# Kernel optimization log

Measured on AMD Instinct MI355X. Metric: run time of the kernel, lower is better.

The kernel has to match this reference:

```python
import jax, jax.numpy as jnp
import numpy as np

N = 50000      # nodes
E = 800000     # edges (avg degree 16)
HID = 64       # hidden / out_channels per head (concat=False)
EDIM = 3       # edge_dim
H = 4          # heads
C = 64         # per-head channels (== hidden since concat=False mean)
L = 2          # ode_layers
NEG_SLOPE = 0.2
LN_EPS = 1e-5


def setup_inputs() -> dict:
    key = jax.random.key(0)
    ks = jax.random.split(key, 12)
    h = jax.random.normal(ks[0], (N, HID), dtype=jnp.float32)
    edge_index = jax.random.randint(ks[1], (2, E), 0, N, dtype=jnp.int64)
    edge_attr = jax.random.normal(ks[2], (E, EDIM), dtype=jnp.float32)
    t = jnp.zeros((), dtype=jnp.float32)
    s = 1.0 / np.sqrt(HID)
    lin_W = jax.random.normal(ks[3], (L, H * C, HID), dtype=jnp.float32) * s
    lin_W = lin_W.at[L - 1].mul(0.1)  # mimics gats[-1].lin.weight.mul_(0.1)
    lin_edge_W = jax.random.normal(ks[4], (L, H * C, EDIM), dtype=jnp.float32) * (1.0 / np.sqrt(EDIM))
    att_src = jax.random.normal(ks[5], (L, H, C), dtype=jnp.float32) * s
    att_dst = jax.random.normal(ks[6], (L, H, C), dtype=jnp.float32) * s
    att_edge = jax.random.normal(ks[7], (L, H, C), dtype=jnp.float32) * s
    bias = jnp.zeros((L, C), dtype=jnp.float32)
    ln_gamma = jnp.ones((L, HID), dtype=jnp.float32)
    ln_beta = jnp.zeros((L, HID), dtype=jnp.float32)
    return {"t": t, "h": h, "edge_index": edge_index, "edge_attr": edge_attr,
            "lin_W": lin_W, "lin_edge_W": lin_edge_W, "att_src": att_src,
            "att_dst": att_dst, "att_edge": att_edge, "bias": bias,
            "ln_gamma": ln_gamma, "ln_beta": ln_beta}


def _gat_layer(z, src, dst, lin_W, lin_edge_W, att_src, att_dst, att_edge,
               bias, edge_attr):
    n = z.shape[0]
    x = (z @ lin_W.T).reshape(n, H, C)                      # [N,H,C]
    a_src = (x * att_src).sum(-1)                            # [N,H]
    a_dst = (x * att_dst).sum(-1)                            # [N,H]
    e = (edge_attr @ lin_edge_W.T).reshape(-1, H, C)         # [E,H,C]
    a_e = (e * att_edge).sum(-1)                             # [E,H]
    alpha = jax.nn.leaky_relu(a_src[src] + a_dst[dst] + a_e, NEG_SLOPE)
    # segment-softmax over incoming edges of each destination node
    amax = jax.ops.segment_max(alpha, dst, num_segments=n)
    amax = jnp.where(jnp.isfinite(amax), amax, 0.0)
    ex = jnp.exp(alpha - amax[dst])                          # [E,H]
    denom = jax.ops.segment_sum(ex, dst, num_segments=n)
    w = ex / (denom[dst] + 1e-16)
    msg = jax.ops.segment_sum(w[:, :, None] * x[src], dst, num_segments=n)
    return msg.mean(axis=1) + bias                           # [N,C] (concat=False)


def reference(t, h, edge_index, edge_attr, lin_W, lin_edge_W, att_src,
              att_dst, att_edge, bias, ln_gamma, ln_beta):
    src, dst = edge_index[0], edge_index[1]
    z = h
    for i in range(L):
        out = _gat_layer(z, src, dst, lin_W[i], lin_edge_W[i], att_src[i],
                         att_dst[i], att_edge[i], bias[i], edge_attr)
        mu = out.mean(-1, keepdims=True)
        var = ((out - mu) ** 2).mean(-1, keepdims=True)
        ln = (out - mu) / jnp.sqrt(var + LN_EPS) * ln_gamma[i] + ln_beta[i]
        z = jax.nn.silu(ln)
    return z
```

## Files before the change

### kernel.cpp

```cpp
#include <hip/hip_runtime.h>
#include <math.h>

#define NN 50000
#define NE 800000
#define NEG_SLOPE 0.2f
#define LN_EPS 1e-5f
#define SROW 264

typedef unsigned short ushort_t;
typedef unsigned int uint_t;
typedef __attribute__((ext_vector_type(8))) short bf16x8;
typedef __attribute__((ext_vector_type(4))) float f32x4;

__device__ __forceinline__ float bf2f(ushort_t u) {
    return __uint_as_float(((uint_t)u) << 16);
}
__device__ __forceinline__ ushort_t f2bf(float f) {
    uint_t b = __float_as_uint(f);
    uint_t r = (b + 0x7fffu + ((b >> 16) & 1u)) >> 16;
    return (ushort_t)r;
}
__device__ __forceinline__ float ldx(const void* p, size_t i, int isbf) {
    return isbf ? bf2f(((const ushort_t*)p)[i]) : ((const float*)p)[i];
}
__device__ __forceinline__ int clampN(int v) {
    return v < 0 ? 0 : (v >= NN ? NN - 1 : v);
}
__device__ __forceinline__ int ld_src(const int* ei, int e, int f64) {
    return clampN(f64 ? ei[2 * e] : ei[e]);
}
__device__ __forceinline__ int ld_dst(const int* ei, int e, int f64) {
    return clampN(f64 ? ei[2 * NE + 2 * e] : ei[NE + e]);
}
__device__ __forceinline__ int sniff_isbf(const void* hptr) {
    const ushort_t* hu = (const ushort_t*)hptr;
    int bf = 1;
    for (int i = 0; i < 512; i += 2) {
        uint_t ex = (hu[i] >> 7) & 0xFFu;
        if (ex > 0x8Cu) bf = 0;
    }
    return bf;
}
__device__ __forceinline__ int sniff_f64(const int* ei) {
    return (ei[1] == 0 && ei[3] == 0 && ei[5] == 0 && ei[7] == 0) ? 1 : 0;
}

__global__ __launch_bounds__(256) void setup(
    const void* __restrict__ lin_W, const void* __restrict__ lin_edge_W,
    const void* __restrict__ att_src, const void* __restrict__ att_dst,
    const void* __restrict__ att_edge, const void* __restrict__ h_in,
    const int* __restrict__ ei, float* __restrict__ Mbuf,
    ushort_t* __restrict__ wext, ushort_t* __restrict__ hbf,
    int* __restrict__ deg, int* __restrict__ flags) {
    int tid = threadIdx.x, lane = tid & 63;
    int nthreads = gridDim.x * 256;
    int gtid = blockIdx.x * 256 + tid;
    __shared__ int s_isbf;
    if (tid == 0) s_isbf = sniff_isbf(h_in);
    __syncthreads();
    int isbf = s_isbf;
    if (gtid == 0) {
        flags[0] = sniff_f64(ei);
        flags[1] = isbf;
    }
    for (int i = gtid; i < NN; i += nthreads) deg[i] = 0;
    if (blockIdx.x == 0) {
        for (int rep = 0; rep < 2; ++rep) {
            int idx = rep * 256 + tid;
            int l = idx >> 8, hc = idx & 255;
            float ae = ldx(att_edge, l * 256 + hc, isbf);
            size_t b3 = ((size_t)l * 256 + hc) * 3;
            float q0 = ae * ldx(lin_edge_W, b3 + 0, isbf);
            float q1 = ae * ldx(lin_edge_W, b3 + 1, isbf);
            float q2 = ae * ldx(lin_edge_W, b3 + 2, isbf);
            for (int off = 32; off > 0; off >>= 1) {
                q0 += __shfl_down(q0, off);
                q1 += __shfl_down(q1, off);
                q2 += __shfl_down(q2, off);
            }
            if (lane == 0) {
                int h = (idx >> 6) & 3;
                Mbuf[(l * 4 + h) * 3 + 0] = q0;
                Mbuf[(l * 4 + h) * 3 + 1] = q1;
                Mbuf[(l * 4 + h) * 3 + 2] = q2;
            }
        }
    }
    for (int idx = gtid; idx < 2 * 272 * 64; idx += nthreads) {
        int d = idx & 63;
        int row = (idx >> 6) % 272;
        int l = idx / (272 * 64);
        float v = 0.f;
        if (row < 256) {
            v = ldx(lin_W, ((size_t)l * 256 + row) * 64 + d, isbf);
        } else if (row < 264) {
            int h = (row - 256) & 3;
            const void* att = (row < 260) ? att_src : att_dst;
            for (int c = 0; c < 64; ++c) {
                v += ldx(lin_W, ((size_t)l * 256 + h * 64 + c) * 64 + d, isbf) *
                     ldx(att, l * 256 + h * 64 + c, isbf);
            }
        }
        wext[((size_t)l * 272 + row) * 64 + d] = f2bf(v);
    }
    if (!isbf) {
        for (int i = gtid; i < NN * 64; i += nthreads)
            hbf[i] = f2bf(((const float*)h_in)[i]);
    }
}


__global__ void csr_hist_pos(const int* __restrict__ ei, int* __restrict__ deg,
                             int* __restrict__ pos, const int* __restrict__ flags) {
    int e = blockIdx.x * 256 + threadIdx.x;
    if (e >= NE) return;
    pos[e] = atomicAdd(&deg[ld_dst(ei, e, flags[0])], 1);
}

__global__ __launch_bounds__(1024) void csr_scan(const int* __restrict__ deg,
                                                 int* __restrict__ rowptr) {
    __shared__ int sh[1024];
    __shared__ int prefix_sh;
    int tid = threadIdx.x;
    int i = blockIdx.x * 1024 + tid;
    int pre = 0;
    for (int k = tid; k < blockIdx.x * 1024; k += 1024) pre += deg[k];
    sh[tid] = pre;
    __syncthreads();
    for (int off = 512; off > 0; off >>= 1) {
        if (tid < off) sh[tid] += sh[tid + off];
        __syncthreads();
    }
    if (tid == 0) prefix_sh = sh[0];
    __syncthreads();
    int prefix = prefix_sh;
    __syncthreads();
    int v = (i < NN) ? deg[i] : 0;
    sh[tid] = v;
    __syncthreads();
    for (int off = 1; off < 1024; off <<= 1) {
        int t = (tid >= off) ? sh[tid - off] : 0;
        __syncthreads();
        sh[tid] += t;
        __syncthreads();
    }
    if (i < NN) rowptr[i] = prefix + sh[tid] - v;
    if (i == 0) rowptr[NN] = NE;
}

__global__ void csr_fill(const int* __restrict__ ei, const void* __restrict__ edge_attr,
                         const int* __restrict__ rowptr, const int* __restrict__ pos,
                         float4* __restrict__ edata, const int* __restrict__ flags) {
    int e = blockIdx.x * 256 + threadIdx.x;
    if (e >= NE) return;
    int f64 = flags[0], isbf = flags[1];
    int s = ld_src(ei, e, f64), d = ld_dst(ei, e, f64);
    float4 ed;
    ed.x = ldx(edge_attr, (size_t)e * 3 + 0, isbf);
    ed.y = ldx(edge_attr, (size_t)e * 3 + 1, isbf);
    ed.z = ldx(edge_attr, (size_t)e * 3 + 2, isbf);
    ed.w = __int_as_float(s);
    edata[rowptr[d] + pos[e]] = ed;
}


__global__ __launch_bounds__(256) void node_linear(
    const void* __restrict__ h_in, const ushort_t* __restrict__ hbf,
    const ushort_t* __restrict__ zbuf, const ushort_t* __restrict__ wext,
    ushort_t* __restrict__ xb, float* __restrict__ a_src, float* __restrict__ a_dst,
    const int* __restrict__ flags, int layer) {
    __shared__ __align__(16) ushort_t st_all[4 * 16 * SROW];
    int isbf = flags[1];
    int tid = threadIdx.x, wv = tid >> 6, lane = tid & 63;
    int q = lane >> 4, mi = lane & 15;
    const ushort_t* zsrc = (layer == 0) ? (isbf ? (const ushort_t*)h_in : hbf) : zbuf;
    const ushort_t* wl = wext + (size_t)layer * 272 * 64;
    bf16x8 wf[34];
#pragma unroll
    for (int t = 0; t < 17; ++t) {
        const ushort_t* wrow = wl + (size_t)(t * 16 + mi) * 64;
        wf[2 * t]     = *(const bf16x8*)(wrow + q * 8);
        wf[2 * t + 1] = *(const bf16x8*)(wrow + 32 + q * 8);
    }
    ushort_t* st = st_all + wv * 16 * SROW;
    int gwave = blockIdx.x * 4 + wv, nwaves = gridDim.x * 4;
    for (int tile = gwave; tile < NN / 16; tile += nwaves) {
        int mbase = tile * 16, mynode = mbase + mi;
        const ushort_t* zrow = zsrc + (size_t)mynode * 64;
        bf16x8 b0 = *(const bf16x8*)(zrow + q * 8);
        bf16x8 b1 = *(const bf16x8*)(zrow + 32 + q * 8);
#pragma unroll
        for (int t = 0; t < 17; ++t) {
            f32x4 acc = {0.f, 0.f, 0.f, 0.f};
            acc = __builtin_amdgcn_mfma_f32_16x16x32_bf16(wf[2 * t], b0, acc, 0, 0, 0);
            acc = __builtin_amdgcn_mfma_f32_16x16x32_bf16(wf[2 * t + 1], b1, acc, 0, 0, 0);
            if (t < 16) {
                ushort4 pk;
                pk.x = f2bf(acc[0]);
                pk.y = f2bf(acc[1]);
                pk.z = f2bf(acc[2]);
                pk.w = f2bf(acc[3]);
                *(ushort4*)(st + mi * SROW + t * 16 + q * 4) = pk;
            } else {
                float4 av;
                av.x = acc[0]; av.y = acc[1]; av.z = acc[2]; av.w = acc[3];
                if (q == 0) *(float4*)(a_src + (size_t)mynode * 4) = av;
                else if (q == 1) *(float4*)(a_dst + (size_t)mynode * 4) = av;
            }
        }
        for (int nn = 0; nn < 16; ++nn) {
            int node = mbase + nn;
            ushort4 pk;
            pk.x = st[nn * SROW + lane];
            pk.y = st[nn * SROW + 64 + lane];
            pk.z = st[nn * SROW + 128 + lane];
            pk.w = st[nn * SROW + 192 + lane];
            *(ushort4*)(xb + (size_t)node * 256 + lane * 4) = pk;
        }
    }
}

__global__ __launch_bounds__(256) void node_aggregate(
    const int* __restrict__ rowptr, const float4* __restrict__ edata,
    const float* __restrict__ a_src, const float* __restrict__ a_dst,
    const ushort_t* __restrict__ xb, const float* __restrict__ Mbuf,
    const void* __restrict__ bias, const void* __restrict__ gamma,
    const void* __restrict__ beta, ushort_t* __restrict__ zout,
    void* __restrict__ outp, const int* __restrict__ flags, int layer, int last) {
    __shared__ float4 wsh[4][64];
    __shared__ int ssh[4][64];
    int isbf = flags[1];
    int wv = threadIdx.x >> 6;
    int lane = threadIdx.x & 63;
    int n = blockIdx.x * 4 + wv;
    float M[12];
#pragma unroll
    for (int i = 0; i < 12; ++i) M[i] = Mbuf[layer * 12 + i];
    float4 ad = *(const float4*)(a_dst + (size_t)n * 4);
    int start = rowptr[n], end = rowptr[n + 1];
    float acc0 = 0.f, acc1 = 0.f, acc2 = 0.f, acc3 = 0.f;
    float den0 = 0.f, den1 = 0.f, den2 = 0.f, den3 = 0.f;
    for (int cb = start; cb < end; cb += 64) {
        int m = end - cb;
        if (m > 64) m = 64;
        if (lane < m) {
            float4 ed = edata[cb + lane];
            int s = __float_as_int(ed.w);
            float4 as4 = *(const float4*)(a_src + (size_t)s * 4);
            float t0 = as4.x + ad.x + ed.x * M[0] + ed.y * M[1] + ed.z * M[2];
            float t1 = as4.y + ad.y + ed.x * M[3] + ed.y * M[4] + ed.z * M[5];
            float t2 = as4.z + ad.z + ed.x * M[6] + ed.y * M[7] + ed.z * M[8];
            float t3 = as4.w + ad.w + ed.x * M[9] + ed.y * M[10] + ed.z * M[11];
            t0 = t0 > 0.f ? t0 : NEG_SLOPE * t0;
            t1 = t1 > 0.f ? t1 : NEG_SLOPE * t1;
            t2 = t2 > 0.f ? t2 : NEG_SLOPE * t2;
            t3 = t3 > 0.f ? t3 : NEG_SLOPE * t3;
            float4 ex;
            ex.x = __expf(fminf(t0, 80.f));
            ex.y = __expf(fminf(t1, 80.f));
            ex.z = __expf(fminf(t2, 80.f));
            ex.w = __expf(fminf(t3, 80.f));
            wsh[wv][lane] = ex;
            ssh[wv][lane] = s;
        } else {
            wsh[wv][lane] = make_float4(0.f, 0.f, 0.f, 0.f);
            ssh[wv][lane] = 0;
        }
        for (int j = 0; j < m; j += 4) {
            int s0 = ssh[wv][j],     s1 = ssh[wv][j + 1];
            int s2 = ssh[wv][j + 2], s3 = ssh[wv][j + 3];
            float4 w0 = wsh[wv][j];
            float4 w1 = wsh[wv][j + 1];
            float4 w2 = wsh[wv][j + 2];
            float4 w3 = wsh[wv][j + 3];
            ushort4 x0 = *(const ushort4*)(xb + (size_t)s0 * 256 + lane * 4);
            ushort4 x1 = *(const ushort4*)(xb + (size_t)s1 * 256 + lane * 4);
            ushort4 x2 = *(const ushort4*)(xb + (size_t)s2 * 256 + lane * 4);
            ushort4 x3 = *(const ushort4*)(xb + (size_t)s3 * 256 + lane * 4);
            acc0 += w0.x * bf2f(x0.x) + w1.x * bf2f(x1.x) +
                    w2.x * bf2f(x2.x) + w3.x * bf2f(x3.x);
            acc1 += w0.y * bf2f(x0.y) + w1.y * bf2f(x1.y) +
                    w2.y * bf2f(x2.y) + w3.y * bf2f(x3.y);
            acc2 += w0.z * bf2f(x0.z) + w1.z * bf2f(x1.z) +
                    w2.z * bf2f(x2.z) + w3.z * bf2f(x3.z);
            acc3 += w0.w * bf2f(x0.w) + w1.w * bf2f(x1.w) +
                    w2.w * bf2f(x2.w) + w3.w * bf2f(x3.w);
            den0 += w0.x + w1.x + w2.x + w3.x;
            den1 += w0.y + w1.y + w2.y + w3.y;
            den2 += w0.z + w1.z + w2.z + w3.z;
            den3 += w0.w + w1.w + w2.w + w3.w;
        }
    }
    float v = ldx(bias, layer * 64 + lane, isbf) +
              0.25f * (acc0 / (den0 + 1e-16f) + acc1 / (den1 + 1e-16f) +
                       acc2 / (den2 + 1e-16f) + acc3 / (den3 + 1e-16f));
    float sum = v;
    for (int off = 1; off < 64; off <<= 1) sum += __shfl_xor(sum, off);
    float mu = sum * (1.f / 64.f);
    float d = v - mu;
    float vv = d * d;
    for (int off = 1; off < 64; off <<= 1) vv += __shfl_xor(vv, off);
    float var = vv * (1.f / 64.f);
    float ln = d * rsqrtf(var + LN_EPS) * ldx(gamma, layer * 64 + lane, isbf) +
               ldx(beta, layer * 64 + lane, isbf);
    float sl = ln / (1.f + __expf(-ln));
    size_t idx = (size_t)n * 64 + lane;
    if (last) {
        if (isbf) ((ushort_t*)outp)[idx] = f2bf(sl);
        else      ((float*)outp)[idx] = sl;
    } else {
        zout[idx] = f2bf(sl);
    }
}

extern "C" void kernel_launch(void* const* d_in, const int* in_sizes, int n_in,
                              void* d_out, int out_size, void* d_ws, size_t ws_size,
                              hipStream_t stream) {
    int off = (in_sizes[0] == 1) ? 1 : 0;
    const void* h_in  = d_in[off + 0];
    const int*  ei    = (const int*)d_in[off + 1];
    const void* eattr = d_in[off + 2];
    const void* linW  = d_in[off + 3];
    const void* linEW = d_in[off + 4];
    const void* attS  = d_in[off + 5];
    const void* attD  = d_in[off + 6];
    const void* attE  = d_in[off + 7];
    const void* bias  = d_in[off + 8];
    const void* gamma = d_in[off + 9];
    const void* beta  = d_in[off + 10];

    char* w = (char*)d_ws;
    size_t o = 0;
    auto alloc = [&](size_t bytes) {
        void* q = w + o;
        o += (bytes + 255) & ~(size_t)255;
        return q;
    };
    int*    flags  = (int*)alloc(8);
    float*  Mbuf   = (float*)alloc(24 * 4);
    ushort_t* wext = (ushort_t*)alloc((size_t)2 * 272 * 64 * 2);
    float*  a_src  = (float*)alloc((size_t)NN * 4 * 4);
    float*  a_dst  = (float*)alloc((size_t)NN * 4 * 4);
    int*    rowptr = (int*)alloc((size_t)(NN + 1) * 4);
    int*    deg    = (int*)alloc((size_t)NN * 4);
    int*    pos    = (int*)alloc((size_t)NE * 4);
    ushort_t* zbuf = (ushort_t*)alloc((size_t)NN * 64 * 2);
    ushort_t* hbf  = (ushort_t*)alloc((size_t)NN * 64 * 2);
    ushort_t* xb   = (ushort_t*)alloc((size_t)NN * 256 * 2);
    float4* edata  = (float4*)alloc((size_t)NE * 16);

    int nb = (NN + 1023) / 1024;
    setup<<<256, 256, 0, stream>>>(linW, linEW, attS, attD, attE, h_in, ei,
                                   Mbuf, wext, hbf, deg, flags);
    csr_hist_pos<<<(NE + 255) / 256, 256, 0, stream>>>(ei, deg, pos, flags);
    csr_scan<<<nb, 1024, 0, stream>>>(deg, rowptr);
    csr_fill<<<(NE + 255) / 256, 256, 0, stream>>>(ei, eattr, rowptr, pos, edata, flags);

    for (int l = 0; l < 2; ++l) {
        node_linear<<<512, 256, 0, stream>>>(h_in, hbf, zbuf, wext, xb,
                                             a_src, a_dst, flags, l);
        node_aggregate<<<NN / 4, 256, 0, stream>>>(rowptr, edata, a_src, a_dst,
                                                   xb, Mbuf, bias, gamma, beta,
                                                   zbuf, d_out, flags, l, l == 1);
    }
}
```

Baseline: 333.7 us.

## Aggregate raw node features before projection, then apply linear weights post-aggregation

```diff
diff --git a/kernel.cpp b/kernel.cpp
--- a/kernel.cpp
+++ b/kernel.cpp
@@ -5,7 +5,6 @@
 #define NE 800000
 #define NEG_SLOPE 0.2f
 #define LN_EPS 1e-5f
-#define SROW 264
 
 typedef unsigned short ushort_t;
 typedef unsigned int uint_t;
@@ -50,8 +49,8 @@
     const void* __restrict__ att_src, const void* __restrict__ att_dst,
     const void* __restrict__ att_edge, const void* __restrict__ h_in,
     const int* __restrict__ ei, float* __restrict__ Mbuf,
-    ushort_t* __restrict__ wext, ushort_t* __restrict__ hbf,
-    int* __restrict__ deg, int* __restrict__ flags) {
+    ushort_t* __restrict__ ubuf, ushort_t* __restrict__ w2,
+    ushort_t* __restrict__ hbf, int* __restrict__ deg, int* __restrict__ flags) {
     int tid = threadIdx.x, lane = tid & 63;
     int nthreads = gridDim.x * 256;
     int gtid = blockIdx.x * 256 + tid;
@@ -86,22 +85,24 @@
             }
         }
     }
-    for (int idx = gtid; idx < 2 * 272 * 64; idx += nthreads) {
-        int d = idx & 63;
-        int row = (idx >> 6) % 272;
-        int l = idx / (272 * 64);
+    for (int idx = gtid; idx < 1024; idx += nthreads) {
+        int l = idx >> 9, j = (idx >> 6) & 7, d = idx & 63;
+        int h = j & 3;
+        const void* att = (j < 4) ? att_src : att_dst;
         float v = 0.f;
-        if (row < 256) {
-            v = ldx(lin_W, ((size_t)l * 256 + row) * 64 + d, isbf);
-        } else if (row < 264) {
-            int h = (row - 256) & 3;
-            const void* att = (row < 260) ? att_src : att_dst;
-            for (int c = 0; c < 64; ++c) {
-                v += ldx(lin_W, ((size_t)l * 256 + h * 64 + c) * 64 + d, isbf) *
-                     ldx(att, l * 256 + h * 64 + c, isbf);
-            }
-        }
-        wext[((size_t)l * 272 + row) * 64 + d] = f2bf(v);
+        for (int c = 0; c < 64; ++c) {
+            v += ldx(lin_W, ((size_t)l * 256 + h * 64 + c) * 64 + d, isbf) *
+                 ldx(att, l * 256 + h * 64 + c, isbf);
+        }
+        ubuf[idx] = f2bf(v);
+    }
+    for (int idx = gtid; idx < 32768; idx += nthreads) {
+        int l = idx >> 14;
+        int rem = idx & 16383;
+        int c = rem >> 8, k = rem & 255;
+        int h = k >> 6, kk = k & 63;
+        float v = 0.25f * ldx(lin_W, ((size_t)l * 256 + h * 64 + c) * 64 + kk, isbf);
+        w2[idx] = f2bf(v);
     }
     if (!isbf) {
         for (int i = gtid; i < NN * 64; i += nthreads)
@@ -164,75 +165,42 @@
 }
 
 
-__global__ __launch_bounds__(256) void node_linear(
+__global__ __launch_bounds__(256) void node_attn(
     const void* __restrict__ h_in, const ushort_t* __restrict__ hbf,
-    const ushort_t* __restrict__ zbuf, const ushort_t* __restrict__ wext,
-    ushort_t* __restrict__ xb, float* __restrict__ a_src, float* __restrict__ a_dst,
+    const ushort_t* __restrict__ zbuf, const ushort_t* __restrict__ ubuf,
+    float* __restrict__ a_src, float* __restrict__ a_dst,
     const int* __restrict__ flags, int layer) {
-    __shared__ __align__(16) ushort_t st_all[4 * 16 * SROW];
+    int idx = blockIdx.x * 256 + threadIdx.x;
+    int n = idx >> 3, j = idx & 7;
+    if (n >= NN) return;
     int isbf = flags[1];
-    int tid = threadIdx.x, wv = tid >> 6, lane = tid & 63;
-    int q = lane >> 4, mi = lane & 15;
     const ushort_t* zsrc = (layer == 0) ? (isbf ? (const ushort_t*)h_in : hbf) : zbuf;
-    const ushort_t* wl = wext + (size_t)layer * 272 * 64;
-    bf16x8 wf[34];
-#pragma unroll
-    for (int t = 0; t < 17; ++t) {
-        const ushort_t* wrow = wl + (size_t)(t * 16 + mi) * 64;
-        wf[2 * t]     = *(const bf16x8*)(wrow + q * 8);
-        wf[2 * t + 1] = *(const bf16x8*)(wrow + 32 + q * 8);
-    }
-    ushort_t* st = st_all + wv * 16 * SROW;
-    int gwave = blockIdx.x * 4 + wv, nwaves = gridDim.x * 4;
-    for (int tile = gwave; tile < NN / 16; tile += nwaves) {
-        int mbase = tile * 16, mynode = mbase + mi;
-        const ushort_t* zrow = zsrc + (size_t)mynode * 64;
-        bf16x8 b0 = *(const bf16x8*)(zrow + q * 8);
-        bf16x8 b1 = *(const bf16x8*)(zrow + 32 + q * 8);
-#pragma unroll
-        for (int t = 0; t < 17; ++t) {
-            f32x4 acc = {0.f, 0.f, 0.f, 0.f};
-            acc = __builtin_amdgcn_mfma_f32_16x16x32_bf16(wf[2 * t], b0, acc, 0, 0, 0);
-            acc = __builtin_amdgcn_mfma_f32_16x16x32_bf16(wf[2 * t + 1], b1, acc, 0, 0, 0);
-            if (t < 16) {
-                ushort4 pk;
-                pk.x = f2bf(acc[0]);
-                pk.y = f2bf(acc[1]);
-                pk.z = f2bf(acc[2]);
-                pk.w = f2bf(acc[3]);
-                *(ushort4*)(st + mi * SROW + t * 16 + q * 4) = pk;
-            } else {
-                float4 av;
-                av.x = acc[0]; av.y = acc[1]; av.z = acc[2]; av.w = acc[3];
-                if (q == 0) *(float4*)(a_src + (size_t)mynode * 4) = av;
-                else if (q == 1) *(float4*)(a_dst + (size_t)mynode * 4) = av;
-            }
-        }
-        for (int nn = 0; nn < 16; ++nn) {
-            int node = mbase + nn;
-            ushort4 pk;
-            pk.x = st[nn * SROW + lane];
-            pk.y = st[nn * SROW + 64 + lane];
-            pk.z = st[nn * SROW + 128 + lane];
-            pk.w = st[nn * SROW + 192 + lane];
-            *(ushort4*)(xb + (size_t)node * 256 + lane * 4) = pk;
-        }
-    }
+    const uint_t* zr = (const uint_t*)(zsrc + (size_t)n * 64);
+    const uint_t* ur = (const uint_t*)(ubuf + ((size_t)layer * 8 + j) * 64);
+    float acc = 0.f;
+#pragma unroll
+    for (int i = 0; i < 32; ++i) {
+        uint_t za = zr[i], ua = ur[i];
+        acc += __uint_as_float(za << 16) * __uint_as_float(ua << 16) +
+               __uint_as_float(za & 0xffff0000u) * __uint_as_float(ua & 0xffff0000u);
+    }
+    if (j < 4) a_src[n * 4 + j] = acc;
+    else       a_dst[n * 4 + (j - 4)] = acc;
 }
 
 __global__ __launch_bounds__(256) void node_aggregate(
     const int* __restrict__ rowptr, const float4* __restrict__ edata,
     const float* __restrict__ a_src, const float* __restrict__ a_dst,
-    const ushort_t* __restrict__ xb, const float* __restrict__ Mbuf,
-    const void* __restrict__ bias, const void* __restrict__ gamma,
-    const void* __restrict__ beta, ushort_t* __restrict__ zout,
-    void* __restrict__ outp, const int* __restrict__ flags, int layer, int last) {
+    const void* __restrict__ h_in, const ushort_t* __restrict__ hbf,
+    const ushort_t* __restrict__ zbuf, const float* __restrict__ Mbuf,
+    ushort_t* __restrict__ t, const int* __restrict__ flags, int layer) {
     __shared__ float4 wsh[4][64];
     __shared__ int ssh[4][64];
     int isbf = flags[1];
     int wv = threadIdx.x >> 6;
     int lane = threadIdx.x & 63;
     int n = blockIdx.x * 4 + wv;
+    const ushort_t* zsrc = (layer == 0) ? (isbf ? (const ushort_t*)h_in : hbf) : zbuf;
     float M[12];
 #pragma unroll
     for (int i = 0; i < 12; ++i) M[i] = Mbuf[layer * 12 + i];
@@ -243,9 +211,11 @@
     for (int cb = start; cb < end; cb += 64) {
         int m = end - cb;
         if (m > 64) m = 64;
+        float4 ex = make_float4(0.f, 0.f, 0.f, 0.f);
+        int s = 0;
         if (lane < m) {
             float4 ed = edata[cb + lane];
-            int s = __float_as_int(ed.w);
+            s = __float_as_int(ed.w);
             float4 as4 = *(const float4*)(a_src + (size_t)s * 4);
             float t0 = as4.x + ad.x + ed.x * M[0] + ed.y * M[1] + ed.z * M[2];
             float t1 = as4.y + ad.y + ed.x * M[3] + ed.y * M[4] + ed.z * M[5];
@@ -255,17 +225,21 @@
             t1 = t1 > 0.f ? t1 : NEG_SLOPE * t1;
             t2 = t2 > 0.f ? t2 : NEG_SLOPE * t2;
             t3 = t3 > 0.f ? t3 : NEG_SLOPE * t3;
-            float4 ex;
             ex.x = __expf(fminf(t0, 80.f));
             ex.y = __expf(fminf(t1, 80.f));
             ex.z = __expf(fminf(t2, 80.f));
             ex.w = __expf(fminf(t3, 80.f));
-            wsh[wv][lane] = ex;
-            ssh[wv][lane] = s;
-        } else {
-            wsh[wv][lane] = make_float4(0.f, 0.f, 0.f, 0.f);
-            ssh[wv][lane] = 0;
-        }
+        }
+        wsh[wv][lane] = ex;
+        ssh[wv][lane] = s;
+        float d0 = ex.x, d1 = ex.y, d2 = ex.z, d3 = ex.w;
+        for (int off = 1; off < 64; off <<= 1) {
+            d0 += __shfl_xor(d0, off);
+            d1 += __shfl_xor(d1, off);
+            d2 += __shfl_xor(d2, off);
+            d3 += __shfl_xor(d3, off);
+        }
+        den0 += d0; den1 += d1; den2 += d2; den3 += d3;
         for (int j = 0; j < m; j += 4) {
             int s0 = ssh[wv][j],     s1 = ssh[wv][j + 1];
             int s2 = ssh[wv][j + 2], s3 = ssh[wv][j + 3];
@@ -273,43 +247,81 @@
             float4 w1 = wsh[wv][j + 1];
             float4 w2 = wsh[wv][j + 2];
             float4 w3 = wsh[wv][j + 3];
-            ushort4 x0 = *(const ushort4*)(xb + (size_t)s0 * 256 + lane * 4);
-            ushort4 x1 = *(const ushort4*)(xb + (size_t)s1 * 256 + lane * 4);
-            ushort4 x2 = *(const ushort4*)(xb + (size_t)s2 * 256 + lane * 4);
-            ushort4 x3 = *(const ushort4*)(xb + (size_t)s3 * 256 + lane * 4);
-            acc0 += w0.x * bf2f(x0.x) + w1.x * bf2f(x1.x) +
-                    w2.x * bf2f(x2.x) + w3.x * bf2f(x3.x);
-            acc1 += w0.y * bf2f(x0.y) + w1.y * bf2f(x1.y) +
-                    w2.y * bf2f(x2.y) + w3.y * bf2f(x3.y);
-            acc2 += w0.z * bf2f(x0.z) + w1.z * bf2f(x1.z) +
-                    w2.z * bf2f(x2.z) + w3.z * bf2f(x3.z);
-            acc3 += w0.w * bf2f(x0.w) + w1.w * bf2f(x1.w) +
-                    w2.w * bf2f(x2.w) + w3.w * bf2f(x3.w);
-            den0 += w0.x + w1.x + w2.x + w3.x;
-            den1 += w0.y + w1.y + w2.y + w3.y;
-            den2 += w0.z + w1.z + w2.z + w3.z;
-            den3 += w0.w + w1.w + w2.w + w3.w;
-        }
-    }
-    float v = ldx(bias, layer * 64 + lane, isbf) +
-              0.25f * (acc0 / (den0 + 1e-16f) + acc1 / (den1 + 1e-16f) +
-                       acc2 / (den2 + 1e-16f) + acc3 / (den3 + 1e-16f));
-    float sum = v;
-    for (int off = 1; off < 64; off <<= 1) sum += __shfl_xor(sum, off);
-    float mu = sum * (1.f / 64.f);
-    float d = v - mu;
-    float vv = d * d;
-    for (int off = 1; off < 64; off <<= 1) vv += __shfl_xor(vv, off);
-    float var = vv * (1.f / 64.f);
-    float ln = d * rsqrtf(var + LN_EPS) * ldx(gamma, layer * 64 + lane, isbf) +
-               ldx(beta, layer * 64 + lane, isbf);
-    float sl = ln / (1.f + __expf(-ln));
-    size_t idx = (size_t)n * 64 + lane;
-    if (last) {
-        if (isbf) ((ushort_t*)outp)[idx] = f2bf(sl);
-        else      ((float*)outp)[idx] = sl;
-    } else {
-        zout[idx] = f2bf(sl);
+            float z0 = bf2f(zsrc[(size_t)s0 * 64 + lane]);
+            float z1 = bf2f(zsrc[(size_t)s1 * 64 + lane]);
+            float z2 = bf2f(zsrc[(size_t)s2 * 64 + lane]);
+            float z3 = bf2f(zsrc[(size_t)s3 * 64 + lane]);
+            acc0 += w0.x * z0 + w1.x * z1 + w2.x * z2 + w3.x * z3;
+            acc1 += w0.y * z0 + w1.y * z1 + w2.y * z2 + w3.y * z3;
+            acc2 += w0.z * z0 + w1.z * z1 + w2.z * z2 + w3.z * z3;
+            acc3 += w0.w * z0 + w1.w * z1 + w2.w * z2 + w3.w * z3;
+        }
+    }
+    size_t tb = (size_t)n * 256 + lane;
+    t[tb]       = f2bf(acc0 / (den0 + 1e-16f));
+    t[tb + 64]  = f2bf(acc1 / (den1 + 1e-16f));
+    t[tb + 128] = f2bf(acc2 / (den2 + 1e-16f));
+    t[tb + 192] = f2bf(acc3 / (den3 + 1e-16f));
+}
+
+__global__ __launch_bounds__(256) void node_post(
+    const ushort_t* __restrict__ t, const ushort_t* __restrict__ w2,
+    const void* __restrict__ bias, const void* __restrict__ gamma,
+    const void* __restrict__ beta, ushort_t* __restrict__ zout,
+    void* __restrict__ outp, const int* __restrict__ flags, int layer, int last) {
+    __shared__ __align__(16) float st_all[4][16][68];
+    int isbf = flags[1];
+    int tid = threadIdx.x, wv = tid >> 6, lane = tid & 63;
+    int q = lane >> 4, mi = lane & 15;
+    const ushort_t* w2l = w2 + (size_t)layer * 64 * 256;
+    bf16x8 af[4][8];
+#pragma unroll
+    for (int ct = 0; ct < 4; ++ct) {
+        const ushort_t* wrow = w2l + (size_t)(ct * 16 + mi) * 256;
+#pragma unroll
+        for (int kt = 0; kt < 8; ++kt)
+            af[ct][kt] = *(const bf16x8*)(wrow + kt * 32 + q * 8);
+    }
+    float bz = ldx(bias, layer * 64 + lane, isbf);
+    float gm = ldx(gamma, layer * 64 + lane, isbf);
+    float bt = ldx(beta, layer * 64 + lane, isbf);
+    int gwave = blockIdx.x * 4 + wv, nwaves = gridDim.x * 4;
+    for (int tile = gwave; tile < NN / 16; tile += nwaves) {
+        int mbase = tile * 16, mynode = mbase + mi;
+        const ushort_t* trow = t + (size_t)mynode * 256;
+        bf16x8 bf[8];
+#pragma unroll
+        for (int kt = 0; kt < 8; ++kt)
+            bf[kt] = *(const bf16x8*)(trow + kt * 32 + q * 8);
+#pragma unroll
+        for (int ct = 0; ct < 4; ++ct) {
+            f32x4 acc = {0.f, 0.f, 0.f, 0.f};
+#pragma unroll
+            for (int kt = 0; kt < 8; ++kt)
+                acc = __builtin_amdgcn_mfma_f32_16x16x32_bf16(af[ct][kt], bf[kt], acc, 0, 0, 0);
+#pragma unroll
+            for (int r = 0; r < 4; ++r)
+                st_all[wv][mi][ct * 16 + q * 4 + r] = acc[r];
+        }
+        for (int nn = 0; nn < 16; ++nn) {
+            float v = st_all[wv][nn][lane] + bz;
+            float sum = v;
+            for (int off = 1; off < 64; off <<= 1) sum += __shfl_xor(sum, off);
+            float mu = sum * (1.f / 64.f);
+            float d = v - mu;
+            float vv = d * d;
+            for (int off = 1; off < 64; off <<= 1) vv += __shfl_xor(vv, off);
+            float var = vv * (1.f / 64.f);
+            float ln = d * rsqrtf(var + LN_EPS) * gm + bt;
+            float sl = ln / (1.f + __expf(-ln));
+            size_t idx = (size_t)(mbase + nn) * 64 + lane;
+            if (last) {
+                if (isbf) ((ushort_t*)outp)[idx] = f2bf(sl);
+                else      ((float*)outp)[idx] = sl;
+            } else {
+                zout[idx] = f2bf(sl);
+            }
+        }
     }
 }
 
@@ -338,7 +350,8 @@
     };
     int*    flags  = (int*)alloc(8);
     float*  Mbuf   = (float*)alloc(24 * 4);
-    ushort_t* wext = (ushort_t*)alloc((size_t)2 * 272 * 64 * 2);
+    ushort_t* ubuf = (ushort_t*)alloc((size_t)2 * 8 * 64 * 2);
+    ushort_t* w2   = (ushort_t*)alloc((size_t)2 * 64 * 256 * 2);
     float*  a_src  = (float*)alloc((size_t)NN * 4 * 4);
     float*  a_dst  = (float*)alloc((size_t)NN * 4 * 4);
     int*    rowptr = (int*)alloc((size_t)(NN + 1) * 4);
@@ -346,21 +359,23 @@
     int*    pos    = (int*)alloc((size_t)NE * 4);
     ushort_t* zbuf = (ushort_t*)alloc((size_t)NN * 64 * 2);
     ushort_t* hbf  = (ushort_t*)alloc((size_t)NN * 64 * 2);
-    ushort_t* xb   = (ushort_t*)alloc((size_t)NN * 256 * 2);
+    ushort_t* tbuf = (ushort_t*)alloc((size_t)NN * 256 * 2);
     float4* edata  = (float4*)alloc((size_t)NE * 16);
 
     int nb = (NN + 1023) / 1024;
     setup<<<256, 256, 0, stream>>>(linW, linEW, attS, attD, attE, h_in, ei,
-                                   Mbuf, wext, hbf, deg, flags);
+                                   Mbuf, ubuf, w2, hbf, deg, flags);
     csr_hist_pos<<<(NE + 255) / 256, 256, 0, stream>>>(ei, deg, pos, flags);
     csr_scan<<<nb, 1024, 0, stream>>>(deg, rowptr);
     csr_fill<<<(NE + 255) / 256, 256, 0, stream>>>(ei, eattr, rowptr, pos, edata, flags);
 
     for (int l = 0; l < 2; ++l) {
-        node_linear<<<512, 256, 0, stream>>>(h_in, hbf, zbuf, wext, xb,
-                                             a_src, a_dst, flags, l);
+        node_attn<<<(NN * 8 + 255) / 256, 256, 0, stream>>>(h_in, hbf, zbuf, ubuf,
+                                                            a_src, a_dst, flags, l);
         node_aggregate<<<NN / 4, 256, 0, stream>>>(rowptr, edata, a_src, a_dst,
-                                                   xb, Mbuf, bias, gamma, beta,
-                                                   zbuf, d_out, flags, l, l == 1);
-    }
-}
+                                                   h_in, hbf, zbuf, Mbuf, tbuf,
+                                                   flags, l);
+        node_post<<<512, 256, 0, stream>>>(tbuf, w2, bias, gamma, beta, zbuf,
+                                           d_out, flags, l, l == 1);
+    }
+}
```

Result: no change. 339.6 us (+1.8%).
